# Optimization experiments

Measured on AMD Instinct MI355X. Metric: run time of the kernel, lower is better.

The kernel has to match this reference:

```python
import jax, jax.numpy as jnp
import numpy as np

E, D, H = 1024, 64, 16   # embed_dim, head_dim, num_heads
B, L = 8, 4096


def _ln(x, g, b, eps=1e-5):
    m = jnp.mean(x, axis=-1, keepdims=True)
    v = jnp.var(x, axis=-1, keepdims=True)
    return (x - m) / jnp.sqrt(v + eps) * g + b


def setup_inputs() -> dict:
    key = jax.random.key(0)
    ks = jax.random.split(key, 10)
    s_e = 1.0 / np.sqrt(E)
    s_d = 1.0 / np.sqrt(D)
    f32 = jnp.float32
    return {
        "emb": jax.random.normal(ks[0], (B, L, E), f32),
        # per-head linears stacked on a leading head axis
        "Wa": jax.random.normal(ks[1], (H, E, D), f32) * s_e,
        "ba": jnp.zeros((H, D), f32),
        "Wb": jax.random.normal(ks[2], (H, E, D), f32) * s_e,
        "bb": jnp.zeros((H, D), f32),
        "Wc": jax.random.normal(ks[3], (H, D, D), f32) * s_d,
        "bc": jnp.zeros((H, D), f32),
        "head_w": jnp.ones((H,), f32),
        "hn_g": jnp.ones((H, D), f32),
        "hn_b": jnp.zeros((H, D), f32),
        "Wd": jax.random.normal(ks[4], (E, D), f32) * s_e,
        "bd": jnp.zeros((D,), f32),
        "W1": jax.random.normal(ks[5], (D, 4 * D), f32) * s_d,
        "b1": jnp.zeros((4 * D,), f32),
        "W2": jax.random.normal(ks[6], (4 * D, D), f32) * (1.0 / np.sqrt(4 * D)),
        "b2": jnp.zeros((D,), f32),
        "Wp": jax.random.normal(ks[7], (D, D), f32) * s_d,
        "bp": jnp.zeros((D,), f32),
        "ng": jnp.ones((D,), f32),
        "nb": jnp.zeros((D,), f32),
    }


def reference(emb, Wa, ba, Wb, bb, Wc, bc, head_w, hn_g, hn_b,
              Wd, bd, W1, b1, W2, b2, Wp, bp, ng, nb):
    b_sz, seq_len, _ = emb.shape
    n_heads, d_head = ba.shape

    # gates depend only on x_t -> precompute for all t, all heads  [B,L,H,D]
    a = jnp.tanh(jnp.einsum('ble,hed->blhd', emb, Wa) + ba)
    bt = jnp.einsum('ble,hed->blhd', emb, Wb) + bb

    # linear recurrence h_t = a_t * h_{t-1} + b_t over time
    a_t = jnp.moveaxis(a, 1, 0)    # [L,B,H,D]
    b_t = jnp.moveaxis(bt, 1, 0)

    def step(h, ab):
        at, btt = ab
        h = at * h + btt
        return h, h

    h0 = jnp.zeros((b_sz, n_heads, d_head), emb.dtype)
    _, hs = jax.lax.scan(step, h0, (a_t, b_t))
    hs = jnp.moveaxis(hs, 0, 1)    # [B,L,H,D]

    dx = emb @ Wd + bd             # [B,L,D] shared D(x_t)

    out = jnp.einsum('blhd,hde->blhe', hs, Wc) + bc + dx[:, :, None, :]
    out = _ln(out, hn_g, hn_b)     # per-head LayerNorm, gamma/beta [H,D]

    sum_heads = dx + jnp.einsum('h,blhd->bld', head_w, out)
    z = sum_heads / n_heads

    u = z + _ln(z, ng, nb)
    ffn = jax.nn.gelu(u @ W1 + b1, approximate=False) @ W2 + b2
    h_out = u + ffn
    return h_out @ Wp + bp
```

## Files before the change

kernel.cpp:

```cpp
#include <hip/hip_runtime.h>
#include <hip/hip_bf16.h>
#include <math.h>
#include <stdint.h>

#define E_DIM 1024
#define D_DIM 64
#define H_DIM 16
#define B_SZ  8
#define L_SEQ 4096
#define M_TOK (B_SZ * L_SEQ)
#define NCAT  2112
#define NPAD  2176
#define CHUNK 128
#define NCHUNK (L_SEQ / CHUNK)

typedef float  f32x4  __attribute__((ext_vector_type(4)));
typedef __bf16 bf16x8 __attribute__((ext_vector_type(8)));
typedef __bf16 bf16x4 __attribute__((ext_vector_type(4)));

__device__ __forceinline__ float tanh_fast(float v) {
  float vc = fminf(fmaxf(v, -12.f), 12.f);
  float ex = __expf(vc + vc);
  return (ex - 1.f) / (ex + 1.f);
}
__device__ __forceinline__ void load_lds16(const void* g, void* l) {
  __builtin_amdgcn_global_load_lds(
      (const __attribute__((address_space(1))) void*)g,
      (__attribute__((address_space(3))) void*)l, 16, 0, 0);
}

__global__ __launch_bounds__(256) void cast_emb(const float* __restrict__ in,
                                                bf16x4* __restrict__ out) {
  int i = blockIdx.x * 256 + threadIdx.x;
  float4 v = ((const float4*)in)[i];
  bf16x4 o;
  o[0] = (__bf16)v.x; o[1] = (__bf16)v.y; o[2] = (__bf16)v.z; o[3] = (__bf16)v.w;
  out[i] = o;
}

__global__ __launch_bounds__(256) void pack_w(
    const float* __restrict__ Wa, const float* __restrict__ ba,
    const float* __restrict__ Wb, const float* __restrict__ bb,
    const float* __restrict__ Wd, const float* __restrict__ bd,
    __bf16* __restrict__ wcat, float* __restrict__ bias) {
  int gid = blockIdx.x * 256 + threadIdx.x;
  int n = gid >> 10, k = gid & 1023;
  float w, bv;
  if (n < 1024) {
    int h = n >> 6, d = n & 63;
    w = Wa[((h << 10) | k) * 64 + d]; bv = ba[n];
  } else if (n < 2048) {
    int nn = n - 1024; int h = nn >> 6, d = nn & 63;
    w = Wb[((h << 10) | k) * 64 + d]; bv = bb[nn];
  } else if (n < NCAT) {
    int d = n - 2048;
    w = Wd[k * 64 + d];  bv = bd[d];
  } else { w = 0.f; bv = 0.f; }
  wcat[n * 1024 + k] = (__bf16)w;
  if (k == 0) bias[n] = bv;
}

__global__ __launch_bounds__(256) void pack_ffnw(
    const float* __restrict__ W1, const float* __restrict__ W2,
    const float* __restrict__ Wp,
    __bf16* __restrict__ g_w1t, __bf16* __restrict__ g_w2t,
    __bf16* __restrict__ g_wpt) {
  int idx = blockIdx.x * 256 + threadIdx.x;
  if (idx < 16384) {
    int k = idx >> 8, n = idx & 255;
    g_w1t[n * 72 + k] = (__bf16)W1[idx];
  } else if (idx < 32768) {
    int j = idx - 16384; int k = j >> 6, n = j & 63;
    g_w2t[n * 256 + (((k >> 3) ^ (n & 7)) << 3) + (k & 7)] = (__bf16)W2[j];
  } else {
    int j = idx - 32768; int k = j >> 6, n = j & 63;
    g_wpt[n * 72 + k] = (__bf16)Wp[j];
  }
}

__global__ __launch_bounds__(256) void pack_wct(const float* __restrict__ Wc,
                                                __bf16* __restrict__ wct) {
  int idx = blockIdx.x * 256 + threadIdx.x;
  int h = idx >> 12, e = (idx >> 6) & 63, d = idx & 63;
  wct[idx] = (__bf16)Wc[h * 4096 + d * 64 + e];
}

__global__ __launch_bounds__(256) void gemm_fused(
    const __bf16* __restrict__ A, const __bf16* __restrict__ Wt,
    const float* __restrict__ bias,
    __bf16* __restrict__ abuf, __bf16* __restrict__ bbuf, float* __restrict__ dxbuf) {
  __shared__ __bf16 As[128 * 64];
  __shared__ __bf16 Bs[128 * 64];
  const int nt = blockIdx.x, mt = blockIdx.y;
  const int m0 = mt * 128, n0 = nt * 128;
  const int t = threadIdx.x, w = t >> 6, l = t & 63;
  const int lr = l >> 3, lc = l & 7;
  const int swz = lc ^ lr;
  const int q = l >> 4, c16 = l & 15;

  f32x4 acc[4][4];
#pragma unroll
  for (int i = 0; i < 4; ++i)
#pragma unroll
    for (int j = 0; j < 4; ++j) acc[i][j] = (f32x4)(0.f);

  const __bf16* gA = A  + (size_t)(m0 + w * 8 + lr) * 1024 + swz * 8;
  const __bf16* gB = Wt + (size_t)(n0 + w * 8 + lr) * 1024 + swz * 8;
  __bf16* lA = As + w * 512;
  __bf16* lB = Bs + w * 512;

  for (int kk = 0; kk < 16; ++kk) {
    const int k0 = kk * 64;
#pragma unroll
    for (int r = 0; r < 4; ++r) {
      load_lds16(gA + (size_t)r * 32 * 1024 + k0, lA + r * 2048);
      load_lds16(gB + (size_t)r * 32 * 1024 + k0, lB + r * 2048);
    }
    __syncthreads();
#pragma unroll
    for (int ks = 0; ks < 2; ++ks) {
      bf16x8 af[4], bfr[4];
#pragma unroll
      for (int i = 0; i < 4; ++i) {
        int mloc = (w >> 1) * 64 + i * 16 + c16;
        int cp = (ks * 4 + q) ^ (mloc & 7);
        af[i] = *(const bf16x8*)(As + mloc * 64 + cp * 8);
      }
#pragma unroll
      for (int j = 0; j < 4; ++j) {
        int nloc = (w & 1) * 64 + j * 16 + c16;
        int cp = (ks * 4 + q) ^ (nloc & 7);
        bfr[j] = *(const bf16x8*)(Bs + nloc * 64 + cp * 8);
      }
#pragma unroll
      for (int i = 0; i < 4; ++i)
#pragma unroll
        for (int j = 0; j < 4; ++j)
          acc[i][j] = __builtin_amdgcn_mfma_f32_16x16x32_bf16(af[i], bfr[j], acc[i][j], 0, 0, 0);
    }
    __syncthreads();
  }

#pragma unroll
  for (int j = 0; j < 4; ++j) {
    int n = n0 + (w & 1) * 64 + j * 16 + c16;
    float bv = bias[n];
#pragma unroll
    for (int i = 0; i < 4; ++i) {
      int mbase = m0 + (w >> 1) * 64 + i * 16 + q * 4;
#pragma unroll
      for (int r = 0; r < 4; ++r) {
        float v = acc[i][j][r] + bv;
        int m = mbase + r;
        if (n < 1024)            abuf[(size_t)m * 1024 + n] = (__bf16)tanh_fast(v);
        else if (n < 2048)       bbuf[(size_t)m * 1024 + (n - 1024)] = (__bf16)v;
        else if (n < NCAT)       dxbuf[m * 64 + (n - 2048)] = v;
      }
    }
  }
}

__global__ __launch_bounds__(256) void scan_local_bf(
    __bf16* __restrict__ abuf, __bf16* __restrict__ bbuf,
    float* __restrict__ cA, float* __restrict__ cH) {
  int bc = blockIdx.x;
  int n4 = threadIdx.x * 4;
  size_t base = (size_t)bc * CHUNK * 1024 + n4;
  float p[4] = {1.f, 1.f, 1.f, 1.f}, h[4] = {0.f, 0.f, 0.f, 0.f};
  for (int s = 0; s < CHUNK; ++s) {
    size_t idx = base + (size_t)s * 1024;
    bf16x4 av = *(const bf16x4*)(abuf + idx);
    bf16x4 bv = *(const bf16x4*)(bbuf + idx);
    bf16x4 po, ho;
#pragma unroll
    for (int i = 0; i < 4; ++i) {
      float a = (float)av[i];
      p[i] *= a;
      h[i] = fmaf(a, h[i], (float)bv[i]);
      po[i] = (__bf16)p[i];
      ho[i] = (__bf16)h[i];
    }
    *(bf16x4*)(abuf + idx) = po;
    *(bf16x4*)(bbuf + idx) = ho;
  }
  int ci = bc * 1024 + n4;
  float4 pv = {p[0], p[1], p[2], p[3]};
  float4 hv = {h[0], h[1], h[2], h[3]};
  *(float4*)(cA + ci) = pv;
  *(float4*)(cH + ci) = hv;
}

__global__ __launch_bounds__(256) void scan_carry(
    const float* __restrict__ cA, const float* __restrict__ cH, float* __restrict__ cIn) {
  int gid = blockIdx.x * 256 + threadIdx.x;
  int n = gid & 1023, b = gid >> 10;
  float carry = 0.f;
  for (int c = 0; c < NCHUNK; ++c) {
    int idx = (b * NCHUNK + c) * 1024 + n;
    cIn[idx] = carry;
    carry = fmaf(cA[idx], carry, cH[idx]);
  }
}

__global__ __launch_bounds__(256) void heads_mfma(
    const __bf16* __restrict__ ahat, const __bf16* __restrict__ hloc,
    const float* __restrict__ dxbuf, const float* __restrict__ cIn,
    const __bf16* __restrict__ wct, const float* __restrict__ bch,
    const float* __restrict__ head_w, const float* __restrict__ hng,
    const float* __restrict__ hnb, const float* __restrict__ ng,
    const float* __restrict__ nbv, float* __restrict__ ubuf) {
  __shared__ float carryS[1024];
  const int tid = threadIdx.x, w = tid >> 6, l = tid & 63;
  const int q = l >> 4, c16 = l & 15;
  const int m0 = blockIdx.x * 64;
  const int b = m0 >> 12, c = (m0 & 4095) >> 7;
  const int cb = (b * NCHUNK + c) * 1024;
  ((float4*)carryS)[tid] = ((const float4*)(cIn + cb))[tid];
  __syncthreads();

  const size_t arow = (size_t)(m0 + w * 16 + c16) * 1024;

  float dxr[4][4];
#pragma unroll
  for (int j = 0; j < 4; ++j)
#pragma unroll
    for (int r = 0; r < 4; ++r)
      dxr[j][r] = dxbuf[(m0 + w * 16 + q * 4 + r) * 64 + j * 16 + c16];

  f32x4 accum[4];
#pragma unroll
  for (int j = 0; j < 4; ++j) accum[j] = (f32x4)(0.f);

  for (int h = 0; h < H_DIM; ++h) {
    bf16x8 af[2];
#pragma unroll
    for (int ks = 0; ks < 2; ++ks) {
      int dbase = h * 64 + ks * 32 + q * 8;
      bf16x8 av = *(const bf16x8*)(ahat + arow + dbase);
      bf16x8 hv = *(const bf16x8*)(hloc + arow + dbase);
      float4 cv0 = *(const float4*)(carryS + dbase);
      float4 cv1 = *(const float4*)(carryS + dbase + 4);
      bf16x8 hf;
      hf[0] = (__bf16)fmaf((float)av[0], cv0.x, (float)hv[0]);
      hf[1] = (__bf16)fmaf((float)av[1], cv0.y, (float)hv[1]);
      hf[2] = (__bf16)fmaf((float)av[2], cv0.z, (float)hv[2]);
      hf[3] = (__bf16)fmaf((float)av[3], cv0.w, (float)hv[3]);
      hf[4] = (__bf16)fmaf((float)av[4], cv1.x, (float)hv[4]);
      hf[5] = (__bf16)fmaf((float)av[5], cv1.y, (float)hv[5]);
      hf[6] = (__bf16)fmaf((float)av[6], cv1.z, (float)hv[6]);
      hf[7] = (__bf16)fmaf((float)av[7], cv1.w, (float)hv[7]);
      af[ks] = hf;
    }
    f32x4 acc[4];
#pragma unroll
    for (int j = 0; j < 4; ++j) acc[j] = (f32x4)(0.f);
#pragma unroll
    for (int ks = 0; ks < 2; ++ks)
#pragma unroll
      for (int j = 0; j < 4; ++j) {
        bf16x8 bf = *(const bf16x8*)(wct + h * 4096 + (j * 16 + c16) * 64 + ks * 32 + q * 8);
        acc[j] = __builtin_amdgcn_mfma_f32_16x16x32_bf16(af[ks], bf, acc[j], 0, 0, 0);
      }
    float hw = head_w[h];
    float g4[4], be4[4], bb4[4];
#pragma unroll
    for (int j = 0; j < 4; ++j) {
      int nh = h * 64 + j * 16 + c16;
      g4[j] = hng[nh]; bb4[j] = hnb[nh]; be4[j] = bch[nh];
    }
#pragma unroll
    for (int r = 0; r < 4; ++r) {
      float v0 = acc[0][r] + be4[0] + dxr[0][r];
      float v1 = acc[1][r] + be4[1] + dxr[1][r];
      float v2 = acc[2][r] + be4[2] + dxr[2][r];
      float v3 = acc[3][r] + be4[3] + dxr[3][r];
      float s  = (v0 + v1) + (v2 + v3);
      float s2 = fmaf(v0, v0, fmaf(v1, v1, fmaf(v2, v2, v3 * v3)));
#pragma unroll
      for (int off = 1; off < 16; off <<= 1) {
        s  += __shfl_xor(s, off, 64);
        s2 += __shfl_xor(s2, off, 64);
      }
      float mean = s * (1.f / 64.f);
      float var  = fmaf(s2, 1.f / 64.f, -mean * mean);
      float inv  = rsqrtf(fmaxf(var, 0.f) + 1e-5f);
      accum[0][r] = fmaf(hw, fmaf((v0 - mean) * inv, g4[0], bb4[0]), accum[0][r]);
      accum[1][r] = fmaf(hw, fmaf((v1 - mean) * inv, g4[1], bb4[1]), accum[1][r]);
      accum[2][r] = fmaf(hw, fmaf((v2 - mean) * inv, g4[2], bb4[2]), accum[2][r]);
      accum[3][r] = fmaf(hw, fmaf((v3 - mean) * inv, g4[3], bb4[3]), accum[3][r]);
    }
  }
  float ng4[4], nb4[4];
#pragma unroll
  for (int j = 0; j < 4; ++j) { ng4[j] = ng[j * 16 + c16]; nb4[j] = nbv[j * 16 + c16]; }
#pragma unroll
  for (int r = 0; r < 4; ++r) {
    float z0 = (dxr[0][r] + accum[0][r]) * (1.f / 16.f);
    float z1 = (dxr[1][r] + accum[1][r]) * (1.f / 16.f);
    float z2 = (dxr[2][r] + accum[2][r]) * (1.f / 16.f);
    float z3 = (dxr[3][r] + accum[3][r]) * (1.f / 16.f);
    float s  = (z0 + z1) + (z2 + z3);
    float s2 = fmaf(z0, z0, fmaf(z1, z1, fmaf(z2, z2, z3 * z3)));
#pragma unroll
    for (int off = 1; off < 16; off <<= 1) {
      s  += __shfl_xor(s, off, 64);
      s2 += __shfl_xor(s2, off, 64);
    }
    float mean = s * (1.f / 64.f);
    float var  = fmaf(s2, 1.f / 64.f, -mean * mean);
    float inv  = rsqrtf(fmaxf(var, 0.f) + 1e-5f);
    int mrow = (m0 + w * 16 + q * 4 + r) * 64;
    ubuf[mrow + 0 * 16 + c16] = z0 + fmaf((z0 - mean) * inv, ng4[0], nb4[0]);
    ubuf[mrow + 1 * 16 + c16] = z1 + fmaf((z1 - mean) * inv, ng4[1], nb4[1]);
    ubuf[mrow + 2 * 16 + c16] = z2 + fmaf((z2 - mean) * inv, ng4[2], nb4[2]);
    ubuf[mrow + 3 * 16 + c16] = z3 + fmaf((z3 - mean) * inv, ng4[3], nb4[3]);
  }
}

__global__ __launch_bounds__(256) void ffn_mfma(
    const float* __restrict__ ubuf,
    const __bf16* __restrict__ g_w1t, const __bf16* __restrict__ g_w2t,
    const __bf16* __restrict__ g_wpt,
    const float* __restrict__ b1, const float* __restrict__ b2,
    const float* __restrict__ bp, float* __restrict__ out) {
  __shared__ __bf16 pool[32768];
  const int tid = threadIdx.x, w = tid >> 6, l = tid & 63;
  const int q = l >> 4, c16 = l & 15;
  const int m0 = blockIdx.x * 64;
  __bf16* Us  = pool;
  __bf16* W1T = pool + 4608;
  __bf16* T1S = pool;
  __bf16* W2T = pool + 16384;
  __bf16* HoS = pool;
  __bf16* WpT = pool + 4608;

#pragma unroll
  for (int r = 0; r < 16; ++r) {
    int idx = r * 256 + tid, m = idx >> 6, e = idx & 63;
    Us[m * 72 + e] = (__bf16)ubuf[(size_t)(m0 + m) * 64 + e];
  }
#pragma unroll
  for (int r = 0; r < 9; ++r)
    load_lds16(g_w1t + (size_t)(r * 256 + tid) * 8,
               (char*)pool + 9216 + (r * 256 + w * 64) * 16);
  __syncthreads();

  f32x4 acc1[16];
#pragma unroll
  for (int j = 0; j < 16; ++j) acc1[j] = (f32x4)(0.f);
#pragma unroll
  for (int ks = 0; ks < 2; ++ks) {
    bf16x8 a = *(const bf16x8*)(Us + (w * 16 + c16) * 72 + ks * 32 + q * 8);
#pragma unroll
    for (int j = 0; j < 16; ++j) {
      bf16x8 b = *(const bf16x8*)(W1T + (j * 16 + c16) * 72 + ks * 32 + q * 8);
      acc1[j] = __builtin_amdgcn_mfma_f32_16x16x32_bf16(a, b, acc1[j], 0, 0, 0);
    }
  }
  __syncthreads();

#pragma unroll
  for (int r = 0; r < 8; ++r)
    load_lds16(g_w2t + (size_t)(r * 256 + tid) * 8,
               (char*)pool + 32768 + (r * 256 + w * 64) * 16);
#pragma unroll
  for (int j = 0; j < 16; ++j) {
    int n = j * 16 + c16;
    float bv = b1[n];
#pragma unroll
    for (int rr = 0; rr < 4; ++rr) {
      int m = w * 16 + q * 4 + rr;
      float x = acc1[j][rr] + bv;
      float g = 0.5f * x * (1.f + erff(x * 0.70710678118654752f));
      T1S[m * 256 + (((n >> 3) ^ (m & 7)) << 3) + (n & 7)] = (__bf16)g;
    }
  }
  __syncthreads();

  f32x4 acc2[4];
#pragma unroll
  for (int j = 0; j < 4; ++j) acc2[j] = (f32x4)(0.f);
  const int arow2 = w * 16 + c16;
#pragma unroll
  for (int ks = 0; ks < 8; ++ks) {
    bf16x8 a = *(const bf16x8*)(T1S + arow2 * 256 + (((ks * 4 + q) ^ (arow2 & 7)) << 3));
#pragma unroll
    for (int j = 0; j < 4; ++j) {
      int brow = j * 16 + c16;
      bf16x8 b = *(const bf16x8*)(W2T + brow * 256 + (((ks * 4 + q) ^ (brow & 7)) << 3));
      acc2[j] = __builtin_amdgcn_mfma_f32_16x16x32_bf16(a, b, acc2[j], 0, 0, 0);
    }
  }
  __syncthreads();

#pragma unroll
  for (int r = 0; r < 2; ++r)
    load_lds16(g_wpt + (size_t)(r * 256 + tid) * 8,
               (char*)pool + 9216 + (r * 256 + w * 64) * 16);
  if (tid < 64)
    load_lds16(g_wpt + (size_t)(512 + tid) * 8, (char*)pool + 9216 + 512 * 16);
#pragma unroll
  for (int j = 0; j < 4; ++j) {
    int e = j * 16 + c16;
    float bv = b2[e];
#pragma unroll
    for (int rr = 0; rr < 4; ++rr) {
      int m = w * 16 + q * 4 + rr;
      float hres = acc2[j][rr] + bv + ubuf[(size_t)(m0 + m) * 64 + e];
      HoS[m * 72 + e] = (__bf16)hres;
    }
  }
  __syncthreads();

  f32x4 acc3[4];
#pragma unroll
  for (int j = 0; j < 4; ++j) acc3[j] = (f32x4)(0.f);
#pragma unroll
  for (int ks = 0; ks < 2; ++ks) {
    bf16x8 a = *(const bf16x8*)(HoS + (w * 16 + c16) * 72 + ks * 32 + q * 8);
#pragma unroll
    for (int j = 0; j < 4; ++j) {
      bf16x8 b = *(const bf16x8*)(WpT + (j * 16 + c16) * 72 + ks * 32 + q * 8);
      acc3[j] = __builtin_amdgcn_mfma_f32_16x16x32_bf16(a, b, acc3[j], 0, 0, 0);
    }
  }
#pragma unroll
  for (int j = 0; j < 4; ++j) {
    int e = j * 16 + c16;
    float bv = bp[e];
#pragma unroll
    for (int rr = 0; rr < 4; ++rr) {
      int m = w * 16 + q * 4 + rr;
      out[(size_t)(m0 + m) * 64 + e] = acc3[j][rr] + bv;
    }
  }
}

extern "C" void kernel_launch(void* const* d_in, const int* in_sizes, int n_in,
                              void* d_out, int out_size, void* d_ws, size_t ws_size,
                              hipStream_t stream) {
  const float* emb    = (const float*)d_in[0];
  const float* Wa     = (const float*)d_in[1];
  const float* ba     = (const float*)d_in[2];
  const float* Wb     = (const float*)d_in[3];
  const float* bb     = (const float*)d_in[4];
  const float* Wc     = (const float*)d_in[5];
  const float* bc     = (const float*)d_in[6];
  const float* head_w = (const float*)d_in[7];
  const float* hn_g   = (const float*)d_in[8];
  const float* hn_b   = (const float*)d_in[9];
  const float* Wd     = (const float*)d_in[10];
  const float* bd     = (const float*)d_in[11];
  const float* W1     = (const float*)d_in[12];
  const float* b1     = (const float*)d_in[13];
  const float* W2     = (const float*)d_in[14];
  const float* b2     = (const float*)d_in[15];
  const float* Wp     = (const float*)d_in[16];
  const float* bp     = (const float*)d_in[17];
  const float* ng     = (const float*)d_in[18];
  const float* nb     = (const float*)d_in[19];
  float* out = (float*)d_out;

  char* wsp = (char*)d_ws;
  size_t off = 0;
  auto alloc = [&](size_t bytes) -> char* {
    char* p = wsp + off;
    off += (bytes + 255) & ~(size_t)255;
    return p;
  };
  __bf16* embh  = (__bf16*)alloc((size_t)M_TOK * E_DIM * 2);
  __bf16* wcat  = (__bf16*)alloc((size_t)NPAD * E_DIM * 2);
  float*  bias  = (float*)alloc((size_t)NPAD * 4);
  __bf16* abuf  = (__bf16*)alloc((size_t)M_TOK * 1024 * 2);
  __bf16* bbuf  = (__bf16*)alloc((size_t)M_TOK * 1024 * 2);
  float*  dxbuf = (float*)alloc((size_t)M_TOK * 64 * 4);
  float*  cA    = (float*)alloc((size_t)256 * 1024 * 4);
  float*  cH    = (float*)alloc((size_t)256 * 1024 * 4);
  float*  cIn   = (float*)alloc((size_t)256 * 1024 * 4);
  float*  ubuf  = (float*)alloc((size_t)M_TOK * 64 * 4);
  __bf16* g_w1t = (__bf16*)alloc((size_t)256 * 72 * 2);
  __bf16* g_w2t = (__bf16*)alloc((size_t)64 * 256 * 2);
  __bf16* g_wpt = (__bf16*)alloc((size_t)64 * 72 * 2);
  __bf16* wct   = (__bf16*)alloc((size_t)H_DIM * 64 * 64 * 2);

  cast_emb<<<dim3(32768), dim3(256), 0, stream>>>(emb, (bf16x4*)embh);
  pack_w<<<dim3(8704), dim3(256), 0, stream>>>(Wa, ba, Wb, bb, Wd, bd, wcat, bias);
  pack_ffnw<<<dim3(144), dim3(256), 0, stream>>>(W1, W2, Wp, g_w1t, g_w2t, g_wpt);
  pack_wct<<<dim3(256), dim3(256), 0, stream>>>(Wc, wct);
  gemm_fused<<<dim3(17, 256), dim3(256), 0, stream>>>(embh, wcat, bias, abuf, bbuf, dxbuf);
  scan_local_bf<<<dim3(256), dim3(256), 0, stream>>>(abuf, bbuf, cA, cH);
  scan_carry<<<dim3(32), dim3(256), 0, stream>>>(cA, cH, cIn);
  heads_mfma<<<dim3(512), dim3(256), 0, stream>>>(abuf, bbuf, dxbuf, cIn, wct, bc,
                                                  head_w, hn_g, hn_b, ng, nb, ubuf);
  ffn_mfma<<<dim3(512), dim3(256), 0, stream>>>(ubuf, g_w1t, g_w2t, g_wpt,
                                                b1, b2, bp, out);
}
```

Baseline: 596.3 us.

## Fuse chunk-local linear scan into GEMM epilogue with interleaved a/b columns

Interleaves the Wa and Wb columns in the packed weight, so each 128-column GEMM tile holds 64 matching (a, b) channel pairs. The local scan over the 128-row chunk then runs in shared memory inside the GEMM epilogue, and the separate scan_local_bf kernel is removed. This drops one full read and write of the large a/b intermediates. The block index is also remapped so tiles sharing an M range land on the same XCD. The cost is more LDS use (about 52KB per block, which lowers occupancy), extra barriers and serial 32-step loops in the epilogue.

```diff
diff --git a/kernel.cpp b/kernel.cpp
--- a/kernel.cpp
+++ b/kernel.cpp
@@ -46,12 +46,10 @@
   int gid = blockIdx.x * 256 + threadIdx.x;
   int n = gid >> 10, k = gid & 1023;
   float w, bv;
-  if (n < 1024) {
-    int h = n >> 6, d = n & 63;
-    w = Wa[((h << 10) | k) * 64 + d]; bv = ba[n];
-  } else if (n < 2048) {
-    int nn = n - 1024; int h = nn >> 6, d = nn & 63;
-    w = Wb[((h << 10) | k) * 64 + d]; bv = bb[nn];
+  if (n < 2048) {
+    int p = n >> 1, h = p >> 6, d = p & 63;
+    if (n & 1) { w = Wb[((h << 10) | k) * 64 + d]; bv = bb[p]; }
+    else       { w = Wa[((h << 10) | k) * 64 + d]; bv = ba[p]; }
   } else if (n < NCAT) {
     int d = n - 2048;
     w = Wd[k * 64 + d];  bv = bd[d];
@@ -85,13 +83,24 @@
   wct[idx] = (__bf16)Wc[h * 4096 + d * 64 + e];
 }
 
-__global__ __launch_bounds__(256) void gemm_fused(
+#define SMEM_BYTES 51968
+__global__ __launch_bounds__(256) void gemm_scan(
     const __bf16* __restrict__ A, const __bf16* __restrict__ Wt,
     const float* __restrict__ bias,
-    __bf16* __restrict__ abuf, __bf16* __restrict__ bbuf, float* __restrict__ dxbuf) {
-  __shared__ __bf16 As[128 * 64];
-  __shared__ __bf16 Bs[128 * 64];
-  const int nt = blockIdx.x, mt = blockIdx.y;
+    __bf16* __restrict__ abuf, __bf16* __restrict__ bbuf, float* __restrict__ dxbuf,
+    float* __restrict__ cA, float* __restrict__ cH) {
+  __shared__ __align__(16) char smem[SMEM_BYTES];
+  __bf16* As = (__bf16*)smem;
+  __bf16* Bs = (__bf16*)(smem + 16384);
+  __bf16* Sa = (__bf16*)smem;
+  float*  Sb = (float*)(smem + 16640);
+  float*  SegA = (float*)(smem + 49920);
+  float*  SegH = (float*)(smem + 49920 + 1024);
+
+  const int bb = blockIdx.x;
+  const int xcd = bb & 7, wv = bb >> 3;
+  const int nt = wv % 17;
+  const int mt = xcd * 32 + wv / 17;
   const int m0 = mt * 128, n0 = nt * 128;
   const int t = threadIdx.x, w = t >> 6, l = t & 63;
   const int lr = l >> 3, lc = l & 7;
@@ -141,53 +150,95 @@
     __syncthreads();
   }
 
-#pragma unroll
-  for (int j = 0; j < 4; ++j) {
-    int n = n0 + (w & 1) * 64 + j * 16 + c16;
-    float bv = bias[n];
-#pragma unroll
-    for (int i = 0; i < 4; ++i) {
-      int mbase = m0 + (w >> 1) * 64 + i * 16 + q * 4;
-#pragma unroll
-      for (int r = 0; r < 4; ++r) {
-        float v = acc[i][j][r] + bv;
-        int m = mbase + r;
-        if (n < 1024)            abuf[(size_t)m * 1024 + n] = (__bf16)tanh_fast(v);
-        else if (n < 2048)       bbuf[(size_t)m * 1024 + (n - 1024)] = (__bf16)v;
-        else if (n < NCAT)       dxbuf[m * 64 + (n - 2048)] = v;
-      }
-    }
-  }
-}
-
-__global__ __launch_bounds__(256) void scan_local_bf(
-    __bf16* __restrict__ abuf, __bf16* __restrict__ bbuf,
-    float* __restrict__ cA, float* __restrict__ cH) {
-  int bc = blockIdx.x;
-  int n4 = threadIdx.x * 4;
-  size_t base = (size_t)bc * CHUNK * 1024 + n4;
-  float p[4] = {1.f, 1.f, 1.f, 1.f}, h[4] = {0.f, 0.f, 0.f, 0.f};
-  for (int s = 0; s < CHUNK; ++s) {
-    size_t idx = base + (size_t)s * 1024;
-    bf16x4 av = *(const bf16x4*)(abuf + idx);
-    bf16x4 bv = *(const bf16x4*)(bbuf + idx);
-    bf16x4 po, ho;
-#pragma unroll
-    for (int i = 0; i < 4; ++i) {
-      float a = (float)av[i];
-      p[i] *= a;
-      h[i] = fmaf(a, h[i], (float)bv[i]);
-      po[i] = (__bf16)p[i];
-      ho[i] = (__bf16)h[i];
-    }
-    *(bf16x4*)(abuf + idx) = po;
-    *(bf16x4*)(bbuf + idx) = ho;
-  }
-  int ci = bc * 1024 + n4;
-  float4 pv = {p[0], p[1], p[2], p[3]};
-  float4 hv = {h[0], h[1], h[2], h[3]};
-  *(float4*)(cA + ci) = pv;
-  *(float4*)(cH + ci) = hv;
+  if (nt < 16) {
+#pragma unroll
+    for (int j = 0; j < 4; ++j) {
+      int nloc = (w & 1) * 64 + j * 16 + c16;
+      float bv = bias[n0 + nloc];
+      int pair = nloc >> 1, isB = nloc & 1;
+#pragma unroll
+      for (int i = 0; i < 4; ++i) {
+        int mbase = (w >> 1) * 64 + i * 16 + q * 4;
+#pragma unroll
+        for (int r = 0; r < 4; ++r) {
+          float v = acc[i][j][r] + bv;
+          int m = mbase + r;
+          if (isB) Sb[pair * 130 + m] = v;
+          else     Sa[pair * 130 + m] = (__bf16)tanh_fast(v);
+        }
+      }
+    }
+    __syncthreads();
+
+    {
+      const int p = t & 63, seg = t >> 6, sb = seg * 32;
+      float pc = 1.f, hh = 0.f;
+#pragma unroll
+      for (int s = 0; s < 32; ++s) {
+        int idx = p * 130 + sb + s;
+        float a = (float)Sa[idx];
+        hh = fmaf(a, hh, Sb[idx]);
+        pc *= a;
+        Sa[idx] = (__bf16)pc;
+        Sb[idx] = hh;
+      }
+      SegA[seg * 64 + p] = pc;
+      SegH[seg * 64 + p] = hh;
+      __syncthreads();
+      if (t < 64) {
+        float P = 1.f, Hc = 0.f;
+#pragma unroll
+        for (int k = 0; k < 4; ++k) {
+          float Ak = SegA[k * 64 + t], Hk = SegH[k * 64 + t];
+          SegA[k * 64 + t] = P;  SegH[k * 64 + t] = Hc;
+          Hc = fmaf(Ak, Hc, Hk); P *= Ak;
+        }
+        cA[mt * 1024 + nt * 64 + t] = P;
+        cH[mt * 1024 + nt * 64 + t] = Hc;
+      }
+      __syncthreads();
+      float Pin = SegA[seg * 64 + p], Hin = SegH[seg * 64 + p];
+#pragma unroll
+      for (int s = 0; s < 32; ++s) {
+        int idx = p * 130 + sb + s;
+        float pl = (float)Sa[idx];
+        Sb[idx] = fmaf(pl, Hin, Sb[idx]);
+        Sa[idx] = (__bf16)(pl * Pin);
+      }
+    }
+    __syncthreads();
+
+    {
+      const int m = t >> 1, half = t & 1;
+      size_t grow = (size_t)(m0 + m) * 1024 + nt * 64 + half * 32;
+#pragma unroll
+      for (int g = 0; g < 4; ++g) {
+        bf16x8 av, hv;
+#pragma unroll
+        for (int k = 0; k < 8; ++k) {
+          int p2 = half * 32 + g * 8 + k;
+          av[k] = Sa[p2 * 130 + m];
+          hv[k] = (__bf16)Sb[p2 * 130 + m];
+        }
+        *(bf16x8*)(abuf + grow + g * 8) = av;
+        *(bf16x8*)(bbuf + grow + g * 8) = hv;
+      }
+    }
+  } else {
+#pragma unroll
+    for (int j = 0; j < 4; ++j) {
+      int n = n0 + (w & 1) * 64 + j * 16 + c16;
+      if (n >= NCAT) continue;
+      float bv = bias[n];
+#pragma unroll
+      for (int i = 0; i < 4; ++i) {
+        int mbase = m0 + (w >> 1) * 64 + i * 16 + q * 4;
+#pragma unroll
+        for (int r = 0; r < 4; ++r)
+          dxbuf[(mbase + r) * 64 + (n - 2048)] = acc[i][j][r] + bv;
+      }
+    }
+  }
 }
 
 __global__ __launch_bounds__(256) void scan_carry(
@@ -487,8 +538,8 @@
   pack_w<<<dim3(8704), dim3(256), 0, stream>>>(Wa, ba, Wb, bb, Wd, bd, wcat, bias);
   pack_ffnw<<<dim3(144), dim3(256), 0, stream>>>(W1, W2, Wp, g_w1t, g_w2t, g_wpt);
   pack_wct<<<dim3(256), dim3(256), 0, stream>>>(Wc, wct);
-  gemm_fused<<<dim3(17, 256), dim3(256), 0, stream>>>(embh, wcat, bias, abuf, bbuf, dxbuf);
-  scan_local_bf<<<dim3(256), dim3(256), 0, stream>>>(abuf, bbuf, cA, cH);
+  gemm_scan<<<dim3(4352), dim3(256), 0, stream>>>(embh, wcat, bias, abuf, bbuf,
+                                                  dxbuf, cA, cH);
   scan_carry<<<dim3(32), dim3(256), 0, stream>>>(cA, cH, cIn);
   heads_mfma<<<dim3(512), dim3(256), 0, stream>>>(abuf, bbuf, dxbuf, cIn, wct, bc,
                                                   head_w, hn_g, hn_b, ng, nb, ubuf);
```

Result: slower. 613.6 us (+2.9%).
